# Optimization experiments

Measured on AMD Instinct MI355X. Metric: run time of the kernel, lower is better.

Reference implementation:

```python
import jax, jax.numpy as jnp
import numpy as np
from jax import lax

DN = ('NCHW', 'OIHW', 'NCHW')

def _conv(x, w, b, pad):
    y = lax.conv_general_dilated(x, w, (1, 1), pad, dimension_numbers=DN)
    return y + b[None, :, None, None]

def _squash(u, eps=1e-8):
    sn = jnp.sum(u * u, axis=1, keepdims=True)  # channel-dim squared norm
    return (sn / (1.0 + sn)) * u / (jnp.sqrt(sn) + eps)

def _expert(x, w_caps, b_caps, w_proj, b_proj):
    # 16 stacked 3x3 capsule convs == one 3x3 conv 128->128 (same concat order)
    u = _conv(x, w_caps, b_caps, 'SAME')
    u = _squash(u)
    return _conv(u, w_proj, b_proj, [(0, 0), (0, 0)])

def _process_gate(x, expert_all, g, top):
    B = x.shape[0]
    x0 = x.mean(axis=(2, 3))                          # [B, C] GAP
    gate_out = jax.nn.softmax(x0 @ g, axis=1)         # [B, E]
    usage = gate_out.sum(0)                           # [E]
    tw, ti = lax.top_k(gate_out, top)                 # [B, top]
    tw = jax.nn.softmax(tw, axis=1)
    sel = expert_all[ti, jnp.arange(B)[:, None]]      # [B, top, C, H, W]
    y = jnp.sum(sel * tw[:, :, None, None, None], axis=1)
    loss = jnp.var(usage, ddof=1) / (usage.mean() ** 2 + 1e-10)
    return y, loss

def setup_inputs() -> dict:
    key = jax.random.key(0)
    ks = jax.random.split(key, 8)
    B, C, H, W, E = 8, 128, 64, 64, 8
    fan_g = 1.0 / np.sqrt(C)
    return {
        'x': jax.random.normal(ks[0], (B, C, H, W), jnp.float32),
        'gate1': jax.random.normal(ks[1], (C, E), jnp.float32) * fan_g,
        'gate2': jax.random.normal(ks[2], (C, E), jnp.float32) * fan_g,
        'gate3': jax.random.normal(ks[3], (C, E), jnp.float32) * fan_g,
        'gate4': jax.random.normal(ks[4], (C, E), jnp.float32) * fan_g,
        'W_caps': jax.random.normal(ks[5], (E, C, C, 3, 3), jnp.float32) * (1.0 / np.sqrt(C * 9)),
        'b_caps': jnp.zeros((E, C), jnp.float32),
        'W_proj': jax.random.normal(ks[6], (E, C, C, 1, 1), jnp.float32) * (1.0 / np.sqrt(C)),
        'b_proj': jnp.zeros((E, C), jnp.float32),
    }

def reference(x, gate1, gate2, gate3, gate4, W_caps, b_caps, W_proj, b_proj):
    top = 2
    # Expert outputs are gate-independent: compute each expert on the full batch once.
    expert_all = jax.vmap(lambda wc, bc, wp, bp: _expert(x, wc, bc, wp, bp))(
        W_caps, b_caps, W_proj, b_proj)      # [E, B, C, H, W]
    y1, l1 = _process_gate(x, expert_all, gate1, top)
    y2, l2 = _process_gate(x, expert_all, gate2, top)
    y3, l3 = _process_gate(x, expert_all, gate3, top)
    y4, l4 = _process_gate(x, expert_all, gate4, top)
    return (y1, y2, y3, y4, l1 + l2 + l3 + l4)
```

## Files before the change

### kernel.cpp

```cpp
#include <hip/hip_runtime.h>
#include <math.h>

#define B_   8
#define C_   128
#define E_   8
#define HW_  4096

typedef unsigned short u16;
typedef unsigned int   u32;
typedef __attribute__((ext_vector_type(8))) short bf16x8;
typedef __attribute__((ext_vector_type(4))) float f32x4;

__device__ __forceinline__ u16 f2bf(float f) {
  u32 u = __float_as_uint(f);
  u32 r = (u + 0x7fffu + ((u >> 16) & 1u)) >> 16;
  return (u16)r;
}
__device__ __forceinline__ float bf2f(u16 h) {
  return __uint_as_float(((u32)h) << 16);
}
__device__ __forceinline__ void gld_lds16(const u16* g, u16* l) {
  __builtin_amdgcn_global_load_lds((const __attribute__((address_space(1))) u32*)g,
                                   (__attribute__((address_space(3))) u32*)(void*)l,
                                   16, 0, 0);
}
#define MFMA(a, b, c) __builtin_amdgcn_mfma_f32_16x16x32_bf16(a, b, c, 0, 0, 0)

__global__ __launch_bounds__(256) void k_gate(const float* __restrict__ x0,
    const float* __restrict__ g1, const float* __restrict__ g2,
    const float* __restrict__ g3, const float* __restrict__ g4,
    float* __restrict__ wmat, int* __restrict__ needed,
    float* __restrict__ lossp) {
  __shared__ float go[4][8][8];
  int t = threadIdx.x;
  int g = t >> 6, b = (t >> 3) & 7, e = t & 7;
  const float* gp = (g == 0) ? g1 : (g == 1) ? g2 : (g == 2) ? g3 : g4;
  const float* xr = x0 + b * C_;
  float s = 0.f;
  for (int c = 0; c < C_; ++c) s += xr[c] * gp[c * E_ + e];
  s *= (1.f / 4096.f);
  go[g][b][e] = s;
  wmat[t] = 0.f;
  if (t < 64) needed[t] = 0;
  __syncthreads();
  if (t < 32) {
    int gg = t >> 3, bb = t & 7;
    float m = -1e30f;
#pragma unroll
    for (int k = 0; k < 8; ++k) m = fmaxf(m, go[gg][bb][k]);
    float tmp[8]; float sum = 0.f;
#pragma unroll
    for (int k = 0; k < 8; ++k) { tmp[k] = expf(go[gg][bb][k] - m); sum += tmp[k]; }
    float inv = 1.f / sum;
#pragma unroll
    for (int k = 0; k < 8; ++k) { tmp[k] *= inv; go[gg][bb][k] = tmp[k]; }
    float v0 = -1.f; int i0 = 0;
#pragma unroll
    for (int k = 0; k < 8; ++k) if (tmp[k] > v0) { v0 = tmp[k]; i0 = k; }
    float v1 = -1.f; int i1 = 0;
#pragma unroll
    for (int k = 0; k < 8; ++k) if (k != i0 && tmp[k] > v1) { v1 = tmp[k]; i1 = k; }
    float e1 = expf(v1 - v0);
    float w0 = 1.f / (1.f + e1), w1 = e1 / (1.f + e1);
    wmat[(gg * 8 + bb) * 8 + i0] = w0;
    wmat[(gg * 8 + bb) * 8 + i1] = w1;
    needed[i0 * 8 + bb] = 1;
    needed[i1 * 8 + bb] = 1;
  }
  __syncthreads();
  if (t == 0) {
    float total = 0.f;
    for (int gg = 0; gg < 4; ++gg) {
      float us[8]; float mean = 0.f;
      for (int k = 0; k < 8; ++k) {
        float u = 0.f;
        for (int bb = 0; bb < 8; ++bb) u += go[gg][bb][k];
        us[k] = u; mean += u;
      }
      mean *= 0.125f;
      float var = 0.f;
      for (int k = 0; k < 8; ++k) { float d = us[k] - mean; var += d * d; }
      var *= (1.f / 7.f);
      total += var / (mean * mean + 1e-10f);
    }
    *lossp = total;
  }
}

__global__ __launch_bounds__(256) void k_prep(const float* __restrict__ x,
    const float* __restrict__ Wc, const float* __restrict__ Wp,
    u16* __restrict__ XTh, u16* __restrict__ XTl,
    u16* __restrict__ Wph, u16* __restrict__ Wpl,
    u16* __restrict__ Pph, u16* __restrict__ Ppl, float* __restrict__ x0) {
  __shared__ float T[64 * 129];
  int blk = blockIdx.x;
  if (blk < 512) {
    int y = blk & 63, b = blk >> 6;
    for (int i = threadIdx.x; i < 128 * 64; i += 256) {
      int ci = i >> 6, xc = i & 63;
      T[xc * 129 + ci] = x[((size_t)(b * 128 + ci)) * HW_ + y * 64 + xc];
    }
    __syncthreads();
    if (threadIdx.x < 128) {
      int ci = threadIdx.x;
      float s = 0.f;
      for (int xc = 0; xc < 64; ++xc) s += T[xc * 129 + ci];
      atomicAdd(&x0[b * 128 + ci], s);
    }
    for (int i = threadIdx.x; i < 64 * 128; i += 256) {
      int xc = i >> 7, ci = i & 127;
      float v = T[xc * 129 + ci];
      u16 h = f2bf(v);
      size_t o = ((size_t)(b * HW_ + y * 64 + xc)) * 128 + ci;
      XTh[o] = h;
      XTl[o] = f2bf(v - bf2f(h));
    }
  } else {
    int gid = (blk - 512) * 256 + threadIdx.x;
    int stride = 1024 * 256;
    const int N1 = 8 * 9 * 2 * 128 * 64;
    for (int g = gid; g < N1; g += stride) {
      int k = g & 63;
      int co = (g >> 6) & 127;
      int ch = (g >> 13) & 1;
      int v = g >> 14;
      int tap = v % 9, e = v / 9;
      int ci = ch * 64 + k;
      float wv = Wc[(((size_t)(e * 128 + co)) * 128 + ci) * 9 + tap];
      u16 h = f2bf(wv), lo = f2bf(wv - bf2f(h));
      int idx = (v * 2 + ch) * 8192 + co * 64 + (k ^ ((co & 7) << 3));
      Wph[idx] = h; Wpl[idx] = lo;
    }
    const int N2 = 8 * 4 * 128 * 32;
    for (int g = gid; g < N2; g += stride) {
      int k = g & 31;
      int co = (g >> 5) & 127;
      int c = (g >> 12) & 3;
      int e = g >> 14;
      int ci = c * 32 + k;
      float wv = Wp[((size_t)(e * 128 + co)) * 128 + ci];
      u16 h = f2bf(wv), lo = f2bf(wv - bf2f(h));
      int idx = (e * 4 + c) * 4096 + co * 32 + (k ^ ((co & 3) << 3));
      Pph[idx] = h; Ppl[idx] = lo;
    }
  }
}

__global__ __launch_bounds__(256, 2) void k_expert(
    const u16* __restrict__ XTh, const u16* __restrict__ XTl,
    const u16* __restrict__ Wph, const u16* __restrict__ Wpl,
    const u16* __restrict__ Pph, const u16* __restrict__ Ppl,
    const float* __restrict__ bcap, const float* __restrict__ bproj,
    const int* __restrict__ needed, const float* __restrict__ wmat,
    float* __restrict__ yout) {
  int e = blockIdx.z, b = blockIdx.y;
  if (!needed[e * 8 + b]) return;
  int tile = blockIdx.x;
  int y0 = tile * 2;

  __shared__ __align__(16) char smem[75264];
  u16* S = (u16*)smem;
  const int Ah = 0, Al = 8192, Bh = 16384, Bl = 24576;
  const int Vh = 0, Vl = 16384, Pt = 32768;
  float* snb = (float*)(smem + 73728);
  float* fb  = (float*)(smem + 74752);

  int tid = threadIdx.x;
  int lane = tid & 63, w = tid >> 6;
  int l15 = lane & 15, l4 = lane >> 4;
  int cob = (w >> 1) * 64, nb = (w & 1) * 64;

  f32x4 zero4 = {0.f, 0.f, 0.f, 0.f};
  f32x4 acc[4][4];
#pragma unroll
  for (int i = 0; i < 4; ++i)
#pragma unroll
    for (int j = 0; j < 4; ++j) acc[i][j] = zero4;

  int sn_ = tid >> 1;
  int kh = (tid & 1) * 4;
  int srow = y0 + (sn_ >> 6);
  int scol = sn_ & 63;

  const u16* WphE = Wph + (size_t)e * 9 * 2 * 8192;
  const u16* WplE = Wpl + (size_t)e * 9 * 2 * 8192;

  for (int tap = 0; tap < 9; ++tap) {
    int dy = tap / 3 - 1, dx = tap % 3 - 1;
    int row = srow + dy, col = scol + dx;
    bool val = ((unsigned)row < 64u) && ((unsigned)col < 64u);
    int gidx = val ? ((b * HW_ + row * 64 + col) * 128) : 0;
    for (int ch = 0; ch < 2; ++ch) {
      __syncthreads();
      const u16* wsh = WphE + (tap * 2 + ch) * 8192;
      const u16* wsl = WplE + (tap * 2 + ch) * 8192;
#pragma unroll
      for (int q = 0; q < 4; ++q) {
        int off = (w * 4 + q) * 512;
        gld_lds16(wsh + off + lane * 8, S + Ah + off);
        gld_lds16(wsl + off + lane * 8, S + Al + off);
      }
      int ci0 = ch * 64;
#pragma unroll
      for (int i = 0; i < 4; ++i) {
        int kg = kh + i;
        uint4 vh4 = {0u, 0u, 0u, 0u}, vl4 = {0u, 0u, 0u, 0u};
        if (val) {
          vh4 = *(const uint4*)(XTh + gidx + ci0 + kg * 8);
          vl4 = *(const uint4*)(XTl + gidx + ci0 + kg * 8);
        }
        int wa = sn_ * 64 + ((kg * 8) ^ ((sn_ & 7) << 3));
        *(uint4*)(S + Bh + wa) = vh4;
        *(uint4*)(S + Bl + wa) = vl4;
      }
      __syncthreads();
#pragma unroll
      for (int ks = 0; ks < 2; ++ks) {
        bf16x8 fah[4], fal[4], fbh[4], fbl[4];
#pragma unroll
        for (int i = 0; i < 4; ++i) {
          int co = cob + i * 16 + l15;
          int ka = (ks * 32 + l4 * 8) ^ ((co & 7) << 3);
          fah[i] = *(const bf16x8*)(S + Ah + co * 64 + ka);
          fal[i] = *(const bf16x8*)(S + Al + co * 64 + ka);
        }
#pragma unroll
        for (int j = 0; j < 4; ++j) {
          int pn = nb + j * 16 + l15;
          int kb = (ks * 32 + l4 * 8) ^ ((pn & 7) << 3);
          fbh[j] = *(const bf16x8*)(S + Bh + pn * 64 + kb);
          fbl[j] = *(const bf16x8*)(S + Bl + pn * 64 + kb);
        }
#pragma unroll
        for (int i = 0; i < 4; ++i)
#pragma unroll
          for (int j = 0; j < 4; ++j) {
            acc[i][j] = MFMA(fah[i], fbh[j], acc[i][j]);
            acc[i][j] = MFMA(fah[i], fbl[j], acc[i][j]);
            acc[i][j] = MFMA(fal[i], fbh[j], acc[i][j]);
          }
      }
    }
  }

#pragma unroll
  for (int i = 0; i < 4; ++i)
#pragma unroll
    for (int r = 0; r < 4; ++r) {
      float bc = bcap[e * 128 + cob + i * 16 + l4 * 4 + r];
#pragma unroll
      for (int j = 0; j < 4; ++j) acc[i][j][r] += bc;
    }

#pragma unroll
  for (int j = 0; j < 4; ++j) {
    float p = 0.f;
#pragma unroll
    for (int i = 0; i < 4; ++i)
#pragma unroll
      for (int r = 0; r < 4; ++r) p += acc[i][j][r] * acc[i][j][r];
    p += __shfl_xor(p, 16);
    p += __shfl_xor(p, 32);
    if (lane < 16) snb[(w >> 1) * 128 + nb + j * 16 + lane] = p;
  }
  __syncthreads();
  if (tid < 128) {
    float s2 = snb[tid] + snb[128 + tid];
    fb[tid] = s2 / ((1.f + s2) * (sqrtf(s2) + 1e-8f));
  }
  __syncthreads();

#pragma unroll
  for (int j = 0; j < 4; ++j) {
    int pn = nb + j * 16 + l15;
    float fj = fb[pn];
#pragma unroll
    for (int i = 0; i < 4; ++i) {
      int co0v = cob + i * 16 + l4 * 4;
      float v0 = acc[i][j][0] * fj, v1 = acc[i][j][1] * fj;
      float v2 = acc[i][j][2] * fj, v3 = acc[i][j][3] * fj;
      u16 h0 = f2bf(v0), h1 = f2bf(v1), h2 = f2bf(v2), h3 = f2bf(v3);
      uint2 hp; hp.x = (u32)h0 | ((u32)h1 << 16); hp.y = (u32)h2 | ((u32)h3 << 16);
      u16 q0 = f2bf(v0 - bf2f(h0)), q1 = f2bf(v1 - bf2f(h1));
      u16 q2 = f2bf(v2 - bf2f(h2)), q3 = f2bf(v3 - bf2f(h3));
      uint2 lp; lp.x = (u32)q0 | ((u32)q1 << 16); lp.y = (u32)q2 | ((u32)q3 << 16);
      int ad = pn * 128 + (co0v ^ ((pn & 7) << 3));
      *(uint2*)(S + Vh + ad) = hp;
      *(uint2*)(S + Vl + ad) = lp;
    }
  }
  __syncthreads();

#pragma unroll
  for (int i = 0; i < 4; ++i)
#pragma unroll
    for (int j = 0; j < 4; ++j) acc[i][j] = zero4;

  for (int sp = 0; sp < 2; ++sp) {
    const u16* Psrc = sp ? Ppl : Pph;
    for (int c = 0; c < 4; ++c) {
      __syncthreads();
      const u16* ps = Psrc + (size_t)(e * 4 + c) * 4096;
#pragma unroll
      for (int q = 0; q < 2; ++q) {
        int off = (w * 2 + q) * 512;
        gld_lds16(ps + off + lane * 8, S + Pt + off);
      }
      __syncthreads();
      bf16x8 af[4], bvh[4], bvl[4];
#pragma unroll
      for (int i = 0; i < 4; ++i) {
        int co = cob + i * 16 + l15;
        int ka = (l4 * 8) ^ ((co & 3) << 3);
        af[i] = *(const bf16x8*)(S + Pt + co * 32 + ka);
      }
#pragma unroll
      for (int j = 0; j < 4; ++j) {
        int pn = nb + j * 16 + l15;
        int kb = (c * 32 + l4 * 8) ^ ((pn & 7) << 3);
        bvh[j] = *(const bf16x8*)(S + Vh + pn * 128 + kb);
        bvl[j] = *(const bf16x8*)(S + Vl + pn * 128 + kb);
      }
      if (sp == 0) {
#pragma unroll
        for (int i = 0; i < 4; ++i)
#pragma unroll
          for (int j = 0; j < 4; ++j) {
            acc[i][j] = MFMA(af[i], bvh[j], acc[i][j]);
            acc[i][j] = MFMA(af[i], bvl[j], acc[i][j]);
          }
      } else {
#pragma unroll
        for (int i = 0; i < 4; ++i)
#pragma unroll
          for (int j = 0; j < 4; ++j)
            acc[i][j] = MFMA(af[i], bvh[j], acc[i][j]);
      }
    }
  }

  int posbase = tile * 128;
  float wg0 = wmat[(0 * 8 + b) * 8 + e];
  float wg1 = wmat[(1 * 8 + b) * 8 + e];
  float wg2 = wmat[(2 * 8 + b) * 8 + e];
  float wg3 = wmat[(3 * 8 + b) * 8 + e];
  float* o0 = yout + (size_t)(0 * 8 + b) * (C_ * HW_);
  float* o1 = yout + (size_t)(1 * 8 + b) * (C_ * HW_);
  float* o2 = yout + (size_t)(2 * 8 + b) * (C_ * HW_);
  float* o3 = yout + (size_t)(3 * 8 + b) * (C_ * HW_);
#pragma unroll
  for (int i = 0; i < 4; ++i)
#pragma unroll
    for (int r = 0; r < 4; ++r) {
      int co = cob + i * 16 + l4 * 4 + r;
      float bp = bproj[e * 128 + co];
      size_t rowo = (size_t)co * HW_ + posbase;
#pragma unroll
      for (int j = 0; j < 4; ++j) {
        int p = nb + j * 16 + l15;
        float v = acc[i][j][r] + bp;
        if (wg0 != 0.f) atomicAdd(o0 + rowo + p, wg0 * v);
        if (wg1 != 0.f) atomicAdd(o1 + rowo + p, wg1 * v);
        if (wg2 != 0.f) atomicAdd(o2 + rowo + p, wg2 * v);
        if (wg3 != 0.f) atomicAdd(o3 + rowo + p, wg3 * v);
      }
    }
}

extern "C" void kernel_launch(void* const* d_in, const int* in_sizes, int n_in,
                              void* d_out, int out_size, void* d_ws, size_t ws_size,
                              hipStream_t stream) {
  const float* x  = (const float*)d_in[0];
  const float* g1 = (const float*)d_in[1];
  const float* g2 = (const float*)d_in[2];
  const float* g3 = (const float*)d_in[3];
  const float* g4 = (const float*)d_in[4];
  const float* Wc = (const float*)d_in[5];
  const float* bc = (const float*)d_in[6];
  const float* Wp = (const float*)d_in[7];
  const float* bp = (const float*)d_in[8];
  float* out = (float*)d_out;

  const size_t XTU  = (size_t)B_ * HW_ * C_;
  const size_t WSU  = (size_t)8 * 9 * 2 * 8192;
  const size_t PSU  = (size_t)8 * 4 * 4096;

  char* p = (char*)d_ws;
  u16* XTh = (u16*)p; p += XTU * 2;
  u16* XTl = (u16*)p; p += XTU * 2;
  u16* Wph = (u16*)p; p += WSU * 2;
  u16* Wpl = (u16*)p; p += WSU * 2;
  u16* Pph = (u16*)p; p += PSU * 2;
  u16* Ppl = (u16*)p; p += PSU * 2;
  float* x0   = (float*)p; p += 1024 * 4;
  float* wmat = (float*)p; p += 256 * 4;
  int*   needed = (int*)p; p += 64 * 4;

  hipMemsetAsync(out, 0, (size_t)4 * B_ * C_ * HW_ * 4, stream);
  hipMemsetAsync(x0, 0, 1024 * 4, stream);

  k_prep<<<dim3(1536), dim3(256), 0, stream>>>(x, Wc, Wp, XTh, XTl, Wph, Wpl,
                                               Pph, Ppl, x0);
  k_gate<<<dim3(1), dim3(256), 0, stream>>>(x0, g1, g2, g3, g4, wmat, needed,
                                            out + (size_t)4 * B_ * C_ * HW_);
  k_expert<<<dim3(32, B_, E_), dim3(256), 0, stream>>>(
      XTh, XTl, Wph, Wpl, Pph, Ppl, bc, bp, needed, wmat, out);
}
```

Before: 347.4 us.

## Double-buffer expert conv with async LDS loads and replace atomic combine with separate pass

The 3x3 conv main loop becomes a 36-stage double-buffered pipeline. Both the weight and activation tiles go straight into LDS via global_load_lds, using interleaved hi/lo bf16 layouts and a zero page for padding, and a partial vmcnt wait lets the next stage's loads overlap the current stage's MFMAs. The projection stage is restructured to the same interleaved layout, and its two split passes are merged into a single 3-MFMA pass. Per-gate atomic adds into the outputs are replaced by plain stores of each expert's output to a workspace buffer, followed by a k_combine kernel that does the weighted top-k sum. This removes atomics and the output memset, at the cost of extra global traffic for the expert buffer and one more launch.

```diff
diff --git a/kernel.cpp b/kernel.cpp
--- a/kernel.cpp
+++ b/kernel.cpp
@@ -90,8 +90,8 @@
 __global__ __launch_bounds__(256) void k_prep(const float* __restrict__ x,
     const float* __restrict__ Wc, const float* __restrict__ Wp,
     u16* __restrict__ XTh, u16* __restrict__ XTl,
-    u16* __restrict__ Wph, u16* __restrict__ Wpl,
-    u16* __restrict__ Pph, u16* __restrict__ Ppl, float* __restrict__ x0) {
+    u16* __restrict__ At, u16* __restrict__ Pt_t,
+    float* __restrict__ x0, u16* __restrict__ zp) {
   __shared__ float T[64 * 129];
   int blk = blockIdx.x;
   if (blk < 512) {
@@ -116,54 +116,53 @@
       XTl[o] = f2bf(v - bf2f(h));
     }
   } else {
+    if (blk == 512 && threadIdx.x < 64) zp[threadIdx.x] = 0;
     int gid = (blk - 512) * 256 + threadIdx.x;
     int stride = 1024 * 256;
-    const int N1 = 8 * 9 * 2 * 128 * 64;
+    const int N1 = 8 * 9 * 4 * 128 * 64;
     for (int g = gid; g < N1; g += stride) {
-      int k = g & 63;
+      int t = g & 7;
+      int sl = (g >> 3) & 7;
       int co = (g >> 6) & 127;
-      int ch = (g >> 13) & 1;
-      int v = g >> 14;
+      int ch = (g >> 13) & 3;
+      int v = g >> 15;
       int tap = v % 9, e = v / 9;
-      int ci = ch * 64 + k;
+      int s = sl ^ (co & 7);
+      int ci = ch * 32 + (s & 3) * 8 + t;
       float wv = Wc[(((size_t)(e * 128 + co)) * 128 + ci) * 9 + tap];
-      u16 h = f2bf(wv), lo = f2bf(wv - bf2f(h));
-      int idx = (v * 2 + ch) * 8192 + co * 64 + (k ^ ((co & 7) << 3));
-      Wph[idx] = h; Wpl[idx] = lo;
-    }
-    const int N2 = 8 * 4 * 128 * 32;
+      u16 h = f2bf(wv);
+      At[g] = (s < 4) ? h : f2bf(wv - bf2f(h));
+    }
+    const int N2 = 8 * 4 * 128 * 64;
     for (int g = gid; g < N2; g += stride) {
-      int k = g & 31;
-      int co = (g >> 5) & 127;
-      int c = (g >> 12) & 3;
-      int e = g >> 14;
-      int ci = c * 32 + k;
+      int t = g & 7;
+      int sl = (g >> 3) & 7;
+      int co = (g >> 6) & 127;
+      int chp = (g >> 13) & 3;
+      int e = g >> 15;
+      int s = sl ^ (co & 7);
+      int ci = chp * 32 + (s & 3) * 8 + t;
       float wv = Wp[((size_t)(e * 128 + co)) * 128 + ci];
-      u16 h = f2bf(wv), lo = f2bf(wv - bf2f(h));
-      int idx = (e * 4 + c) * 4096 + co * 32 + (k ^ ((co & 3) << 3));
-      Pph[idx] = h; Ppl[idx] = lo;
+      u16 h = f2bf(wv);
+      Pt_t[g] = (s < 4) ? h : f2bf(wv - bf2f(h));
     }
   }
 }
 
 __global__ __launch_bounds__(256, 2) void k_expert(
     const u16* __restrict__ XTh, const u16* __restrict__ XTl,
-    const u16* __restrict__ Wph, const u16* __restrict__ Wpl,
-    const u16* __restrict__ Pph, const u16* __restrict__ Ppl,
+    const u16* __restrict__ At, const u16* __restrict__ Pt_t,
     const float* __restrict__ bcap, const float* __restrict__ bproj,
-    const int* __restrict__ needed, const float* __restrict__ wmat,
-    float* __restrict__ yout) {
+    const int* __restrict__ needed, const u16* __restrict__ zp,
+    float* __restrict__ expb) {
   int e = blockIdx.z, b = blockIdx.y;
   if (!needed[e * 8 + b]) return;
   int tile = blockIdx.x;
-  int y0 = tile * 2;
-
-  __shared__ __align__(16) char smem[75264];
+
+  __shared__ __align__(16) char smem[81920];
   u16* S = (u16*)smem;
-  const int Ah = 0, Al = 8192, Bh = 16384, Bl = 24576;
-  const int Vh = 0, Vl = 16384, Pt = 32768;
-  float* snb = (float*)(smem + 73728);
-  float* fb  = (float*)(smem + 74752);
+  float* snb = (float*)(smem + 65536);
+  float* fb  = (float*)(smem + 66560);
 
   int tid = threadIdx.x;
   int lane = tid & 63, w = tid >> 6;
@@ -177,70 +176,67 @@
 #pragma unroll
     for (int j = 0; j < 4; ++j) acc[i][j] = zero4;
 
-  int sn_ = tid >> 1;
-  int kh = (tid & 1) * 4;
-  int srow = y0 + (sn_ >> 6);
-  int scol = sn_ & 63;
-
-  const u16* WphE = Wph + (size_t)e * 9 * 2 * 8192;
-  const u16* WplE = Wpl + (size_t)e * 9 * 2 * 8192;
-
-  for (int tap = 0; tap < 9; ++tap) {
+  auto STAGE = [&](int st, int buf) {
+    int tap = st >> 2, ch = st & 3;
+    const u16* Ab = At + (size_t)((e * 9 + tap) * 4 + ch) * 8192;
+#pragma unroll
+    for (int q = 0; q < 4; ++q) {
+      int m = w * 4 + q;
+      gld_lds16(Ab + m * 512 + lane * 8, S + buf + m * 512);
+    }
     int dy = tap / 3 - 1, dx = tap % 3 - 1;
-    int row = srow + dy, col = scol + dx;
-    bool val = ((unsigned)row < 64u) && ((unsigned)col < 64u);
-    int gidx = val ? ((b * HW_ + row * 64 + col) * 128) : 0;
-    for (int ch = 0; ch < 2; ++ch) {
-      __syncthreads();
-      const u16* wsh = WphE + (tap * 2 + ch) * 8192;
-      const u16* wsl = WplE + (tap * 2 + ch) * 8192;
-#pragma unroll
-      for (int q = 0; q < 4; ++q) {
-        int off = (w * 4 + q) * 512;
-        gld_lds16(wsh + off + lane * 8, S + Ah + off);
-        gld_lds16(wsl + off + lane * 8, S + Al + off);
+#pragma unroll
+    for (int q = 0; q < 4; ++q) {
+      int m = w * 4 + q;
+      int pn = m * 8 + (lane >> 3);
+      int sv = (lane & 7) ^ (pn & 7);
+      int gy = tile * 2 + (pn >> 6) + dy;
+      int gx = (pn & 63) + dx;
+      bool val = ((unsigned)gy < 64u) && ((unsigned)gx < 64u);
+      int go_ = ((b << 12) + gy * 64 + gx) * 128 + ch * 32 + (sv & 3) * 8;
+      const u16* src = val ? ((sv < 4 ? XTh : XTl) + go_) : zp;
+      gld_lds16(src, S + buf + 8192 + m * 512);
+    }
+  };
+
+  STAGE(0, 0);
+  for (int s = 0; s < 36; ++s) {
+    int cur = (s & 1) * 16384;
+    if (s < 35) {
+      STAGE(s + 1, ((s + 1) & 1) * 16384);
+      asm volatile("s_waitcnt vmcnt(8)" ::: "memory");
+    } else {
+      asm volatile("s_waitcnt vmcnt(0)" ::: "memory");
+    }
+    __builtin_amdgcn_s_barrier();
+    __builtin_amdgcn_sched_barrier(0);
+    bf16x8 fah[4], fal[4], fbh[4], fbl[4];
+#pragma unroll
+    for (int i = 0; i < 4; ++i) {
+      int co = cob + i * 16 + l15;
+      int sa = (l4 ^ (co & 7)) * 8;
+      fah[i] = *(const bf16x8*)(S + cur + co * 64 + sa);
+      fal[i] = *(const bf16x8*)(S + cur + co * 64 + (sa ^ 32));
+    }
+#pragma unroll
+    for (int j = 0; j < 4; ++j) {
+      int pn = nb + j * 16 + l15;
+      int sb = (l4 ^ (pn & 7)) * 8;
+      fbh[j] = *(const bf16x8*)(S + cur + 8192 + pn * 64 + sb);
+      fbl[j] = *(const bf16x8*)(S + cur + 8192 + pn * 64 + (sb ^ 32));
+    }
+    __builtin_amdgcn_s_setprio(1);
+#pragma unroll
+    for (int i = 0; i < 4; ++i)
+#pragma unroll
+      for (int j = 0; j < 4; ++j) {
+        acc[i][j] = MFMA(fah[i], fbh[j], acc[i][j]);
+        acc[i][j] = MFMA(fah[i], fbl[j], acc[i][j]);
+        acc[i][j] = MFMA(fal[i], fbh[j], acc[i][j]);
       }
-      int ci0 = ch * 64;
-#pragma unroll
-      for (int i = 0; i < 4; ++i) {
-        int kg = kh + i;
-        uint4 vh4 = {0u, 0u, 0u, 0u}, vl4 = {0u, 0u, 0u, 0u};
-        if (val) {
-          vh4 = *(const uint4*)(XTh + gidx + ci0 + kg * 8);
-          vl4 = *(const uint4*)(XTl + gidx + ci0 + kg * 8);
-        }
-        int wa = sn_ * 64 + ((kg * 8) ^ ((sn_ & 7) << 3));
-        *(uint4*)(S + Bh + wa) = vh4;
-        *(uint4*)(S + Bl + wa) = vl4;
-      }
-      __syncthreads();
-#pragma unroll
-      for (int ks = 0; ks < 2; ++ks) {
-        bf16x8 fah[4], fal[4], fbh[4], fbl[4];
-#pragma unroll
-        for (int i = 0; i < 4; ++i) {
-          int co = cob + i * 16 + l15;
-          int ka = (ks * 32 + l4 * 8) ^ ((co & 7) << 3);
-          fah[i] = *(const bf16x8*)(S + Ah + co * 64 + ka);
-          fal[i] = *(const bf16x8*)(S + Al + co * 64 + ka);
-        }
-#pragma unroll
-        for (int j = 0; j < 4; ++j) {
-          int pn = nb + j * 16 + l15;
-          int kb = (ks * 32 + l4 * 8) ^ ((pn & 7) << 3);
-          fbh[j] = *(const bf16x8*)(S + Bh + pn * 64 + kb);
-          fbl[j] = *(const bf16x8*)(S + Bl + pn * 64 + kb);
-        }
-#pragma unroll
-        for (int i = 0; i < 4; ++i)
-#pragma unroll
-          for (int j = 0; j < 4; ++j) {
-            acc[i][j] = MFMA(fah[i], fbh[j], acc[i][j]);
-            acc[i][j] = MFMA(fah[i], fbl[j], acc[i][j]);
-            acc[i][j] = MFMA(fal[i], fbh[j], acc[i][j]);
-          }
-      }
-    }
+    __builtin_amdgcn_s_setprio(0);
+    __builtin_amdgcn_sched_barrier(0);
+    __builtin_amdgcn_s_barrier();
   }
 
 #pragma unroll
@@ -274,9 +270,10 @@
   for (int j = 0; j < 4; ++j) {
     int pn = nb + j * 16 + l15;
     float fj = fb[pn];
+    int prow = pn * 64;
 #pragma unroll
     for (int i = 0; i < 4; ++i) {
-      int co0v = cob + i * 16 + l4 * 4;
+      int cobase = cob + i * 16;
       float v0 = acc[i][j][0] * fj, v1 = acc[i][j][1] * fj;
       float v2 = acc[i][j][2] * fj, v3 = acc[i][j][3] * fj;
       u16 h0 = f2bf(v0), h1 = f2bf(v1), h2 = f2bf(v2), h3 = f2bf(v3);
@@ -284,9 +281,11 @@
       u16 q0 = f2bf(v0 - bf2f(h0)), q1 = f2bf(v1 - bf2f(h1));
       u16 q2 = f2bf(v2 - bf2f(h2)), q3 = f2bf(v3 - bf2f(h3));
       uint2 lp; lp.x = (u32)q0 | ((u32)q1 << 16); lp.y = (u32)q2 | ((u32)q3 << 16);
-      int ad = pn * 128 + (co0v ^ ((pn & 7) << 3));
-      *(uint2*)(S + Vh + ad) = hp;
-      *(uint2*)(S + Vl + ad) = lp;
+      int chp = cobase >> 5;
+      int kg = ((cobase >> 3) + (l4 >> 1)) & 3;
+      int ad = chp * 8192 + prow + (kg ^ (pn & 7)) * 8 + (l4 & 1) * 4;
+      *(uint2*)(S + ad) = hp;
+      *(uint2*)(S + (ad ^ 32)) = lp;
     }
   }
   __syncthreads();
@@ -296,58 +295,44 @@
 #pragma unroll
     for (int j = 0; j < 4; ++j) acc[i][j] = zero4;
 
-  for (int sp = 0; sp < 2; ++sp) {
-    const u16* Psrc = sp ? Ppl : Pph;
-    for (int c = 0; c < 4; ++c) {
-      __syncthreads();
-      const u16* ps = Psrc + (size_t)(e * 4 + c) * 4096;
-#pragma unroll
-      for (int q = 0; q < 2; ++q) {
-        int off = (w * 2 + q) * 512;
-        gld_lds16(ps + off + lane * 8, S + Pt + off);
+  for (int chp = 0; chp < 4; ++chp) {
+    const u16* Pb = Pt_t + (size_t)(e * 4 + chp) * 8192;
+#pragma unroll
+    for (int q = 0; q < 4; ++q) {
+      int m = w * 4 + q;
+      gld_lds16(Pb + m * 512 + lane * 8, S + 32768 + m * 512);
+    }
+    __syncthreads();
+    bf16x8 afh[4], afl[4], bvh[4], bvl[4];
+#pragma unroll
+    for (int i = 0; i < 4; ++i) {
+      int co = cob + i * 16 + l15;
+      int sa = (l4 ^ (co & 7)) * 8;
+      afh[i] = *(const bf16x8*)(S + 32768 + co * 64 + sa);
+      afl[i] = *(const bf16x8*)(S + 32768 + co * 64 + (sa ^ 32));
+    }
+#pragma unroll
+    for (int j = 0; j < 4; ++j) {
+      int pn = nb + j * 16 + l15;
+      int sb = (l4 ^ (pn & 7)) * 8;
+      bvh[j] = *(const bf16x8*)(S + chp * 8192 + pn * 64 + sb);
+      bvl[j] = *(const bf16x8*)(S + chp * 8192 + pn * 64 + (sb ^ 32));
+    }
+    __builtin_amdgcn_s_setprio(1);
+#pragma unroll
+    for (int i = 0; i < 4; ++i)
+#pragma unroll
+      for (int j = 0; j < 4; ++j) {
+        acc[i][j] = MFMA(afh[i], bvh[j], acc[i][j]);
+        acc[i][j] = MFMA(afh[i], bvl[j], acc[i][j]);
+        acc[i][j] = MFMA(afl[i], bvh[j], acc[i][j]);
       }
-      __syncthreads();
-      bf16x8 af[4], bvh[4], bvl[4];
-#pragma unroll
-      for (int i = 0; i < 4; ++i) {
-        int co = cob + i * 16 + l15;
-        int ka = (l4 * 8) ^ ((co & 3) << 3);
-        af[i] = *(const bf16x8*)(S + Pt + co * 32 + ka);
-      }
-#pragma unroll
-      for (int j = 0; j < 4; ++j) {
-        int pn = nb + j * 16 + l15;
-        int kb = (c * 32 + l4 * 8) ^ ((pn & 7) << 3);
-        bvh[j] = *(const bf16x8*)(S + Vh + pn * 128 + kb);
-        bvl[j] = *(const bf16x8*)(S + Vl + pn * 128 + kb);
-      }
-      if (sp == 0) {
-#pragma unroll
-        for (int i = 0; i < 4; ++i)
-#pragma unroll
-          for (int j = 0; j < 4; ++j) {
-            acc[i][j] = MFMA(af[i], bvh[j], acc[i][j]);
-            acc[i][j] = MFMA(af[i], bvl[j], acc[i][j]);
-          }
-      } else {
-#pragma unroll
-        for (int i = 0; i < 4; ++i)
-#pragma unroll
-          for (int j = 0; j < 4; ++j)
-            acc[i][j] = MFMA(af[i], bvh[j], acc[i][j]);
-      }
-    }
+    __builtin_amdgcn_s_setprio(0);
+    __syncthreads();
   }
 
   int posbase = tile * 128;
-  float wg0 = wmat[(0 * 8 + b) * 8 + e];
-  float wg1 = wmat[(1 * 8 + b) * 8 + e];
-  float wg2 = wmat[(2 * 8 + b) * 8 + e];
-  float wg3 = wmat[(3 * 8 + b) * 8 + e];
-  float* o0 = yout + (size_t)(0 * 8 + b) * (C_ * HW_);
-  float* o1 = yout + (size_t)(1 * 8 + b) * (C_ * HW_);
-  float* o2 = yout + (size_t)(2 * 8 + b) * (C_ * HW_);
-  float* o3 = yout + (size_t)(3 * 8 + b) * (C_ * HW_);
+  float* ob = expb + ((size_t)((e * 8 + b) * 128)) * HW_;
 #pragma unroll
   for (int i = 0; i < 4; ++i)
 #pragma unroll
@@ -356,15 +341,37 @@
       float bp = bproj[e * 128 + co];
       size_t rowo = (size_t)co * HW_ + posbase;
 #pragma unroll
-      for (int j = 0; j < 4; ++j) {
-        int p = nb + j * 16 + l15;
-        float v = acc[i][j][r] + bp;
-        if (wg0 != 0.f) atomicAdd(o0 + rowo + p, wg0 * v);
-        if (wg1 != 0.f) atomicAdd(o1 + rowo + p, wg1 * v);
-        if (wg2 != 0.f) atomicAdd(o2 + rowo + p, wg2 * v);
-        if (wg3 != 0.f) atomicAdd(o3 + rowo + p, wg3 * v);
-      }
-    }
+      for (int j = 0; j < 4; ++j)
+        ob[rowo + nb + j * 16 + l15] = acc[i][j][r] + bp;
+    }
+}
+
+__global__ __launch_bounds__(256) void k_combine(const float* __restrict__ expb,
+    const float* __restrict__ wmat, float* __restrict__ yout) {
+  int b = blockIdx.y;
+  float wg[4][8];
+#pragma unroll
+  for (int g = 0; g < 4; ++g)
+#pragma unroll
+    for (int e = 0; e < 8; ++e) wg[g][e] = wmat[(g * 8 + b) * 8 + e];
+  const int NV = C_ * HW_ / 4;
+  for (int i = blockIdx.x * 256 + threadIdx.x; i < NV; i += gridDim.x * 256) {
+    float4 a0 = {0.f, 0.f, 0.f, 0.f}, a1 = a0, a2 = a0, a3 = a0;
+#pragma unroll
+    for (int e = 0; e < 8; ++e) {
+      float w0 = wg[0][e], w1 = wg[1][e], w2 = wg[2][e], w3 = wg[3][e];
+      if (w0 == 0.f && w1 == 0.f && w2 == 0.f && w3 == 0.f) continue;
+      float4 v = ((const float4*)(expb + (size_t)(e * 8 + b) * (C_ * HW_)))[i];
+      a0.x += w0 * v.x; a0.y += w0 * v.y; a0.z += w0 * v.z; a0.w += w0 * v.w;
+      a1.x += w1 * v.x; a1.y += w1 * v.y; a1.z += w1 * v.z; a1.w += w1 * v.w;
+      a2.x += w2 * v.x; a2.y += w2 * v.y; a2.z += w2 * v.z; a2.w += w2 * v.w;
+      a3.x += w3 * v.x; a3.y += w3 * v.y; a3.z += w3 * v.z; a3.w += w3 * v.w;
+    }
+    ((float4*)(yout + (size_t)(0 * 8 + b) * (C_ * HW_)))[i] = a0;
+    ((float4*)(yout + (size_t)(1 * 8 + b) * (C_ * HW_)))[i] = a1;
+    ((float4*)(yout + (size_t)(2 * 8 + b) * (C_ * HW_)))[i] = a2;
+    ((float4*)(yout + (size_t)(3 * 8 + b) * (C_ * HW_)))[i] = a3;
+  }
 }
 
 extern "C" void kernel_launch(void* const* d_in, const int* in_sizes, int n_in,
@@ -381,28 +388,29 @@
   const float* bp = (const float*)d_in[8];
   float* out = (float*)d_out;
 
+  const size_t EXPF = (size_t)E_ * B_ * C_ * HW_;
   const size_t XTU  = (size_t)B_ * HW_ * C_;
-  const size_t WSU  = (size_t)8 * 9 * 2 * 8192;
-  const size_t PSU  = (size_t)8 * 4 * 4096;
+  const size_t ATU  = (size_t)8 * 9 * 4 * 128 * 64;
+  const size_t PTU  = (size_t)8 * 4 * 128 * 64;
 
   char* p = (char*)d_ws;
-  u16* XTh = (u16*)p; p += XTU * 2;
-  u16* XTl = (u16*)p; p += XTU * 2;
-  u16* Wph = (u16*)p; p += WSU * 2;
-  u16* Wpl = (u16*)p; p += WSU * 2;
-  u16* Pph = (u16*)p; p += PSU * 2;
-  u16* Ppl = (u16*)p; p += PSU * 2;
+  float* expb = (float*)p; p += EXPF * 4;
+  u16* XTh  = (u16*)p; p += XTU * 2;
+  u16* XTl  = (u16*)p; p += XTU * 2;
+  u16* At   = (u16*)p; p += ATU * 2;
+  u16* Pt_t = (u16*)p; p += PTU * 2;
   float* x0   = (float*)p; p += 1024 * 4;
   float* wmat = (float*)p; p += 256 * 4;
   int*   needed = (int*)p; p += 64 * 4;
-
-  hipMemsetAsync(out, 0, (size_t)4 * B_ * C_ * HW_ * 4, stream);
+  u16*   zp = (u16*)p;     p += 128;
+
   hipMemsetAsync(x0, 0, 1024 * 4, stream);
 
-  k_prep<<<dim3(1536), dim3(256), 0, stream>>>(x, Wc, Wp, XTh, XTl, Wph, Wpl,
-                                               Pph, Ppl, x0);
+  k_prep<<<dim3(1536), dim3(256), 0, stream>>>(x, Wc, Wp, XTh, XTl, At, Pt_t,
+                                               x0, zp);
   k_gate<<<dim3(1), dim3(256), 0, stream>>>(x0, g1, g2, g3, g4, wmat, needed,
                                             out + (size_t)4 * B_ * C_ * HW_);
   k_expert<<<dim3(32, B_, E_), dim3(256), 0, stream>>>(
-      XTh, XTl, Wph, Wpl, Pph, Ppl, bc, bp, needed, wmat, out);
-}
+      XTh, XTl, At, Pt_t, bc, bp, needed, zp, expb);
+  k_combine<<<dim3(128, B_), dim3(256), 0, stream>>>(expb, wmat, out);
+}
```

New measurement: 290.0 us. 1.2x faster.
